# Optimization experiments

Hardware: AMD Instinct MI355X
Metric: run time of the kernel (lower is better)

The kernel has to match this reference:

```python
import jax, jax.numpy as jnp
import numpy as np

L, H, Q, D, N, DFF = 8, 4, 64, 512, 2048, 2048


def setup_inputs() -> dict:
    key = jax.random.key(0)
    ks = jax.random.split(key, 7)
    # Scale params by ~1/sqrt(fan_in) so the 8-layer residual stack stays numerically sane.
    X = jax.random.normal(ks[0], (D, N), dtype=jnp.float32)
    K = jax.random.normal(ks[1], (L, H, Q, D), dtype=jnp.float32) * (1.0 / np.sqrt(D))
    V = jax.random.normal(ks[2], (L, H, D, D), dtype=jnp.float32) * (0.5 / np.sqrt(D))
    W1 = jax.random.normal(ks[3], (L, DFF, D), dtype=jnp.float32) * (1.0 / np.sqrt(D))
    b1 = jax.random.normal(ks[4], (L, DFF, 1), dtype=jnp.float32) * 0.02
    W2 = jax.random.normal(ks[5], (L, D, DFF), dtype=jnp.float32) * (1.0 / np.sqrt(DFF))
    b2 = jax.random.normal(ks[6], (L, D, 1), dtype=jnp.float32) * 0.02
    return {"X": X, "K": K, "V": V, "W1": W1, "b1": b1, "W2": W2, "b2": b2}


def _argmax_attn_all_heads(Kl, Vl, X):
    # Kl: [H,Q,D], Vl: [H,D,D], X: [D,N]
    KX = jnp.einsum('hqd,dn->hqn', Kl, X)                 # [H,Q,N]
    scores = jnp.einsum('hqn,hqm->hnm', KX, KX)           # [H,N,N]
    max_vals = jnp.max(scores, axis=2, keepdims=True)     # [H,N,1]
    mask = (scores >= max_vals - 0.5).astype(X.dtype)     # hard argmax-threshold mask
    row_sums = jnp.maximum(jnp.sum(mask, axis=2, keepdims=True), 1.0)
    active = (jnp.abs(max_vals) > 0.5).astype(X.dtype)
    weights = (mask / row_sums) * active                  # [H,N,N]
    Xw = jnp.einsum('dn,hnm->hdm', X, weights)            # X @ weights per head
    return jnp.einsum('hde,hem->dm', Vl, Xw)              # sum over heads of V @ (X @ weights)


def reference(X, K, V, W1, b1, W2, b2):
    for li in range(L):
        attn = X + _argmax_attn_all_heads(K[li], V[li], X)
        ff1 = jax.nn.relu(W1[li] @ attn + b1[li])
        X = attn + W2[li] @ ff1 + b2[li]
    return X
```

## Files before the change

kernel.cpp:

```cpp
#include <hip/hip_runtime.h>

#define LL   8
#define HH   4
#define QQ   64
#define DD   512
#define NN   2048
#define DFFC 2048
#define ENTRY_CAP (1 << 17)
#define CHUNK 8
#define APPLY_BLOCKS 2048
#define LCAP 2048

typedef short     bf16x8 __attribute__((ext_vector_type(8)));
typedef float     f32x4  __attribute__((ext_vector_type(4)));
typedef unsigned short u16;

__device__ inline void splitf(float v, u16& h, u16& l)
{
    unsigned u  = __float_as_uint(v);
    unsigned uh = u + (0x7FFFu + ((u >> 16) & 1u));
    h = (u16)(uh >> 16);
    float fh = __uint_as_float(((unsigned)h) << 16);
    float r  = v - fh;
    unsigned ur = __float_as_uint(r);
    unsigned ul = ur + (0x7FFFu + ((ur >> 16) & 1u));
    l = (u16)(ul >> 16);
}

__device__ inline unsigned mapf(float f)
{
    unsigned u = __float_as_uint(f);
    return (u >> 31) ? ~u : (u | 0x80000000u);
}
__device__ inline float unmapf(unsigned u)
{
    return (u >> 31) ? __uint_as_float(u ^ 0x80000000u) : __uint_as_float(~u);
}

template <int BIAS, int RELU, int WF32, int WSPLIT>
__global__ __launch_bounds__(512, 2) void mgemm8_k(
    const u16* __restrict__ Ahi, const u16* __restrict__ Alo,
    const u16* __restrict__ Bhi, const u16* __restrict__ Blo,
    float* __restrict__ C, u16* __restrict__ Chi, u16* __restrict__ Clo,
    const float* __restrict__ bias,
    int K, int lda, int ldb, int ldc,
    long sAoff, long sBoff, long sCoff)
{
    __shared__ __align__(16) u16 smem[2 * 2048 * 8];

    const int bz = blockIdx.z;
    Ahi += bz * sAoff;  Alo += bz * sAoff;
    Bhi += bz * sBoff;  Blo += bz * sBoff;
    const long cOff = (long)bz * sCoff;

    const int gx = gridDim.x, nwg = gx * gridDim.y;
    int lin = blockIdx.y * gx + blockIdx.x;
    lin = (lin & 7) * (nwg >> 3) + (lin >> 3);
    const int bx = lin % gx, by = lin / gx;

    const int tid  = threadIdx.x;
    const int lane = tid & 63;
    const int wave = tid >> 6;
    const int quad = lane >> 4, l15 = lane & 15;
    const int wy = wave >> 1, wx = wave & 1;
    const long mTile = (long)by * 128;
    const long nTile = (long)bx * 128;

    const int fsw = (l15 & 3) ^ ((l15 >> 2) & 3);
    const int cA  = (quad ^ fsw) * 8;

    const int sr = tid >> 2;
    const int sc = (tid & 3) ^ ((sr & 3) ^ ((sr >> 2) & 3));
    const long aoff = (mTile + sr) * (long)lda + sc * 8;
    const long boff = (nTile + sr) * (long)ldb + sc * 8;

#define STAGE8(bufi, koff)                                                    \
    {                                                                         \
        u16* lb = (u16*)smem + (bufi) * (2048 * 8) + tid * 8;                 \
        __builtin_amdgcn_global_load_lds(                                     \
            (const __attribute__((address_space(1))) void*)(Ahi + aoff + (koff)), \
            (__attribute__((address_space(3))) void*)(lb), 16, 0, 0);         \
        __builtin_amdgcn_global_load_lds(                                     \
            (const __attribute__((address_space(1))) void*)(Alo + aoff + (koff)), \
            (__attribute__((address_space(3))) void*)(lb + 512 * 8), 16, 0, 0); \
        __builtin_amdgcn_global_load_lds(                                     \
            (const __attribute__((address_space(1))) void*)(Bhi + boff + (koff)), \
            (__attribute__((address_space(3))) void*)(lb + 1024 * 8), 16, 0, 0); \
        __builtin_amdgcn_global_load_lds(                                     \
            (const __attribute__((address_space(1))) void*)(Blo + boff + (koff)), \
            (__attribute__((address_space(3))) void*)(lb + 1536 * 8), 16, 0, 0); \
    }

    f32x4 acc[2][4];
#pragma unroll
    for (int i = 0; i < 2; i++)
#pragma unroll
        for (int j = 0; j < 4; j++)
            acc[i][j] = (f32x4){0.f, 0.f, 0.f, 0.f};

    STAGE8(0, 0)
    int buf = 0;
    const int NT = K >> 5;
    for (int t = 0; t < NT; t++) {
        __syncthreads();
        if (t + 1 < NT) STAGE8(buf ^ 1, (t + 1) << 5)

        const u16* Lb = (const u16*)smem + buf * (2048 * 8);
        bf16x8 ah[2], al[2], bh[4], bl[4];
#pragma unroll
        for (int i = 0; i < 2; i++) {
            const int off = (wy * 32 + i * 16 + l15) * 32 + cA;
            ah[i] = *(const bf16x8*)(Lb + off);
            al[i] = *(const bf16x8*)(Lb + 512 * 8 + off);
        }
#pragma unroll
        for (int j = 0; j < 4; j++) {
            const int off = (wx * 64 + j * 16 + l15) * 32 + cA;
            bh[j] = *(const bf16x8*)(Lb + 1024 * 8 + off);
            bl[j] = *(const bf16x8*)(Lb + 1536 * 8 + off);
        }

#pragma unroll
        for (int i = 0; i < 2; i++)
#pragma unroll
            for (int j = 0; j < 4; j++) {
                acc[i][j] = __builtin_amdgcn_mfma_f32_16x16x32_bf16(
                    ah[i], bh[j], acc[i][j], 0, 0, 0);
                acc[i][j] = __builtin_amdgcn_mfma_f32_16x16x32_bf16(
                    ah[i], bl[j], acc[i][j], 0, 0, 0);
                acc[i][j] = __builtin_amdgcn_mfma_f32_16x16x32_bf16(
                    al[i], bh[j], acc[i][j], 0, 0, 0);
            }
        buf ^= 1;
    }
#undef STAGE8

    const int mBase = (int)mTile + wy * 32;
    const int nBase = (int)nTile + wx * 64;
#pragma unroll
    for (int i = 0; i < 2; i++) {
#pragma unroll
        for (int j = 0; j < 4; j++) {
            const int n = nBase + j * 16 + l15;
            const float bv = BIAS ? bias[n] : 0.0f;
#pragma unroll
            for (int r = 0; r < 4; r++) {
                const int m = mBase + i * 16 + quad * 4 + r;
                float v = acc[i][j][r] + bv;
                if (RELU) v = fmaxf(v, 0.0f);
                const long o = cOff + (long)m * ldc + n;
                if (WF32) C[o] = v;
                if (WSPLIT) {
                    u16 h, l;
                    splitf(v, h, l);
                    Chi[o] = h;
                    Clo[o] = l;
                }
            }
        }
    }
}

template <int MI, int BIAS, int RELU, int WF32, int WSPLIT>
__global__ __launch_bounds__(256, 2) void mgemm_k(
    const u16* __restrict__ Ahi, const u16* __restrict__ Alo,
    const u16* __restrict__ Bhi, const u16* __restrict__ Blo,
    float* __restrict__ C, u16* __restrict__ Chi, u16* __restrict__ Clo,
    const float* __restrict__ bias,
    int M, int N, int K, int lda, int ldb, int ldc,
    long sAoff, long sBoff, long sCoff)
{
    constexpr int ACH = MI * 128;
    constexpr int TOT = 2 * ACH + 1024;
    __shared__ __align__(16) u16 smem[2 * TOT * 8];

    const int bz = blockIdx.z;
    Ahi += bz * sAoff;  Alo += bz * sAoff;
    Bhi += bz * sBoff;  Blo += bz * sBoff;
    const long cOff = (long)bz * sCoff;

    const int gx = gridDim.x, nwg = gx * gridDim.y;
    int lin = blockIdx.y * gx + blockIdx.x;
    lin = (lin & 7) * (nwg >> 3) + (lin >> 3);
    const int bxs = lin % gx, bys = lin / gx;

    const int tid  = threadIdx.x;
    const int wave = tid >> 6, lane = tid & 63;
    const int quad = lane >> 4, l15 = lane & 15;
    const int wy = wave >> 1, wx = wave & 1;
    const long mTile = (long)bys * (MI * 32);
    const long nTile = (long)bxs * 128;
    const int mBase = (int)mTile + wy * (MI * 16);
    const int nBase = (int)nTile + wx * 64;

    const int fsw = (l15 & 3) ^ ((l15 >> 2) & 3);
    const int cA  = (quad ^ fsw) * 8;

#define STAGE(bufi, koff)                                                     \
    {                                                                         \
        _Pragma("unroll")                                                     \
        for (int s = 0; s < TOT / 256; s++) {                                 \
            const int idx = s * 256 + tid;                                    \
            const u16* sp;  long rowb;  int ldx;  int rel;                    \
            if (idx < ACH)                { sp = Ahi; rel = idx;               rowb = 0; ldx = lda; } \
            else if (idx < 2 * ACH)       { sp = Alo; rel = idx - ACH;         rowb = 0; ldx = lda; } \
            else if (idx < 2 * ACH + 512) { sp = Bhi; rel = idx - 2 * ACH;     rowb = 1; ldx = ldb; } \
            else                          { sp = Blo; rel = idx - 2*ACH - 512; rowb = 1; ldx = ldb; } \
            const long rb = rowb ? nTile : mTile;                             \
            const int r = rel >> 2;                                           \
            const int c = (rel & 3) ^ ((r & 3) ^ ((r >> 2) & 3));             \
            const u16* g = sp + (rb + r) * (long)ldx + (koff) + c * 8;        \
            u16* lp = (u16*)smem + (bufi) * (TOT * 8) + idx * 8;              \
            __builtin_amdgcn_global_load_lds(                                 \
                (const __attribute__((address_space(1))) void*)g,             \
                (__attribute__((address_space(3))) void*)lp, 16, 0, 0);       \
        }                                                                     \
    }

    f32x4 acc[MI][4];
#pragma unroll
    for (int i = 0; i < MI; i++)
#pragma unroll
        for (int j = 0; j < 4; j++)
            acc[i][j] = (f32x4){0.f, 0.f, 0.f, 0.f};

    STAGE(0, 0)
    int buf = 0;
    const int NT = K >> 5;
    for (int t = 0; t < NT; t++) {
        __syncthreads();
        if (t + 1 < NT) STAGE(buf ^ 1, (t + 1) << 5)

        const u16* Lb = (const u16*)smem + buf * (TOT * 8);
        bf16x8 ah[MI], al[MI], bh[4], bl[4];
#pragma unroll
        for (int i = 0; i < MI; i++) {
            const int off = (wy * (MI * 16) + i * 16 + l15) * 32 + cA;
            ah[i] = *(const bf16x8*)(Lb + off);
            al[i] = *(const bf16x8*)(Lb + ACH * 8 + off);
        }
#pragma unroll
        for (int j = 0; j < 4; j++) {
            const int off = (wx * 64 + j * 16 + l15) * 32 + cA;
            bh[j] = *(const bf16x8*)(Lb + 2 * ACH * 8 + off);
            bl[j] = *(const bf16x8*)(Lb + 2 * ACH * 8 + 512 * 8 + off);
        }

#pragma unroll
        for (int i = 0; i < MI; i++)
#pragma unroll
            for (int j = 0; j < 4; j++) {
                acc[i][j] = __builtin_amdgcn_mfma_f32_16x16x32_bf16(
                    ah[i], bh[j], acc[i][j], 0, 0, 0);
                acc[i][j] = __builtin_amdgcn_mfma_f32_16x16x32_bf16(
                    ah[i], bl[j], acc[i][j], 0, 0, 0);
                acc[i][j] = __builtin_amdgcn_mfma_f32_16x16x32_bf16(
                    al[i], bh[j], acc[i][j], 0, 0, 0);
            }
        buf ^= 1;
    }
#undef STAGE

#pragma unroll
    for (int i = 0; i < MI; i++) {
#pragma unroll
        for (int j = 0; j < 4; j++) {
            const int n = nBase + j * 16 + l15;
            const float bv = BIAS ? bias[n] : 0.0f;
#pragma unroll
            for (int r = 0; r < 4; r++) {
                const int m = mBase + i * 16 + quad * 4 + r;
                float v = acc[i][j][r] + bv;
                if (RELU) v = fmaxf(v, 0.0f);
                const long o = cOff + (long)m * ldc + n;
                if (WF32) C[o] = v;
                if (WSPLIT) {
                    u16 h, l;
                    splitf(v, h, l);
                    Chi[o] = h;
                    Clo[o] = l;
                }
            }
        }
    }
}

__global__ __launch_bounds__(256, 2) void smax_k(
    const u16* __restrict__ Ghi, const u16* __restrict__ Glo,
    unsigned* __restrict__ rowmaxU, unsigned* __restrict__ tmaxU)
{
    __shared__ __align__(16) u16 gs[4096 * 8];
    const int h = blockIdx.z;
    const int lda = HH * QQ;
    const u16* Gh = Ghi + h * QQ;
    const u16* Gl = Glo + h * QQ;

    const int gx = gridDim.x, nwg = gx * gridDim.y;
    int lin = blockIdx.y * gx + blockIdx.x;
    lin = (lin & 7) * (nwg >> 3) + (lin >> 3);
    const int bxs = lin % gx, bys = lin / gx;

    const int tid  = threadIdx.x;
    const int wave = tid >> 6, lane = tid & 63;
    const int quad = lane >> 4, l15 = lane & 15;
    const int wy = wave >> 1, wx = wave & 1;
    const int rT = bys * 128, cT = bxs * 128;
    const int rB = rT + wy * 64;

#define SSTG(src, rowbase, dstbase)                                           \
    _Pragma("unroll")                                                         \
    for (int it = 0; it < 4; it++) {                                          \
        const int idx = it * 256 + tid;                                       \
        const int r = idx >> 3;                                               \
        const int c = (idx & 7) ^ (r & 7);                                    \
        __builtin_amdgcn_global_load_lds(                                     \
            (const __attribute__((address_space(1))) void*)(src + (long)((rowbase) + r) * lda + c * 8), \
            (__attribute__((address_space(3))) void*)((u16*)gs + (dstbase) + idx * 8), 16, 0, 0); \
    }
    SSTG(Gh, rT, 0)
    SSTG(Gl, rT, 8192)
    SSTG(Gh, cT, 16384)
    SSTG(Gl, cT, 24576)
#undef SSTG
    __syncthreads();

    bf16x8 ah[2][4], al[2][4], bh[2][4], bl[2][4];
#pragma unroll
    for (int s = 0; s < 2; s++) {
#pragma unroll
        for (int i = 0; i < 4; i++) {
            const int ra = wy * 64 + i * 16 + l15;
            const int ca = ((s * 4 + quad) ^ (ra & 7)) * 8;
            ah[s][i] = *(const bf16x8*)(gs + ra * 64 + ca);
            al[s][i] = *(const bf16x8*)(gs + 8192 + ra * 64 + ca);
            const int rb = wx * 64 + i * 16 + l15;
            const int cb = ((s * 4 + quad) ^ (rb & 7)) * 8;
            bh[s][i] = *(const bf16x8*)(gs + 16384 + rb * 64 + cb);
            bl[s][i] = *(const bf16x8*)(gs + 24576 + rb * 64 + cb);
        }
    }

    f32x4 acc[4][4];
#pragma unroll
    for (int i = 0; i < 4; i++)
#pragma unroll
        for (int j = 0; j < 4; j++)
            acc[i][j] = (f32x4){0.f, 0.f, 0.f, 0.f};

#pragma unroll
    for (int s = 0; s < 2; s++)
#pragma unroll
        for (int i = 0; i < 4; i++)
#pragma unroll
            for (int j = 0; j < 4; j++) {
                acc[i][j] = __builtin_amdgcn_mfma_f32_16x16x32_bf16(ah[s][i], bh[s][j], acc[i][j], 0, 0, 0);
                acc[i][j] = __builtin_amdgcn_mfma_f32_16x16x32_bf16(ah[s][i], bl[s][j], acc[i][j], 0, 0, 0);
                acc[i][j] = __builtin_amdgcn_mfma_f32_16x16x32_bf16(al[s][i], bh[s][j], acc[i][j], 0, 0, 0);
            }

    const unsigned tBase = (unsigned)((((h << 4) + bys) << 4) + bxs) * 128u;
#pragma unroll
    for (int i = 0; i < 4; i++)
#pragma unroll
        for (int r = 0; r < 4; r++) {
            float mx = acc[i][0][r];
#pragma unroll
            for (int j = 1; j < 4; j++) mx = fmaxf(mx, acc[i][j][r]);
#pragma unroll
            for (int off = 1; off < 16; off <<= 1)
                mx = fmaxf(mx, __shfl_xor(mx, off, 64));
            if (l15 == 0) {
                const int lr = wy * 64 + i * 16 + quad * 4 + r;
                const unsigned mv = mapf(mx);
                atomicMax(&rowmaxU[h * NN + rT + lr], mv);
                atomicMax(&tmaxU[tBase + lr], mv);
            }
        }
}

__global__ __launch_bounds__(256) void sextract_k(
    const u16* __restrict__ Ghi, const u16* __restrict__ Glo,
    const unsigned* __restrict__ rowmaxU, const unsigned* __restrict__ tmaxU,
    int* __restrict__ rowcnt,
    unsigned int* __restrict__ entries, int* __restrict__ counter)
{
    const int h = blockIdx.z;
    const u16* Ah = Ghi + h * QQ;
    const u16* Al = Glo + h * QQ;
    const int lda = HH * QQ;

    const int gx = gridDim.x, nwg = gx * gridDim.y;
    int lin = blockIdx.y * gx + blockIdx.x;
    lin = (lin & 7) * (nwg >> 3) + (lin >> 3);
    const int bxs = lin % gx, bys = lin / gx;

    const int tid  = threadIdx.x;
    const int wave = tid >> 6, lane = tid & 63;
    const int quad = lane >> 4, l15 = lane & 15;
    const int wy = wave >> 1, wx = wave & 1;
    const int rB = bys * 128 + wy * 64;
    const int cB = bxs * 128 + wx * 64;

    __shared__ float thrS[128];
    __shared__ unsigned lbuf[LCAP];
    __shared__ int lcnt, gbase, anyf;
    if (tid == 0) { lcnt = 0; anyf = 0; }
    if (tid < 128) {
        float mx = unmapf(rowmaxU[h * NN + bys * 128 + tid]);
        float thr = (fabsf(mx) > 0.5f) ? mx - 0.5f : 3.402823466e38f;
        thrS[tid] = thr;
        float tm = unmapf(tmaxU[(unsigned)((((h << 4) + bys) << 4) + bxs) * 128u + tid]);
        if (tm >= thr) atomicAdd(&anyf, 1);
    }
    __syncthreads();
    if (anyf == 0) return;

    bf16x8 ah[2][4], al[2][4], bh[2][4], bl[2][4];
#pragma unroll
    for (int s = 0; s < 2; s++) {
        const int kk = s * 32 + quad * 8;
#pragma unroll
        for (int i = 0; i < 4; i++) {
            long ar = (long)(rB + i * 16 + l15) * lda + kk;
            ah[s][i] = *(const bf16x8*)(Ah + ar);
            al[s][i] = *(const bf16x8*)(Al + ar);
            long br = (long)(cB + i * 16 + l15) * lda + kk;
            bh[s][i] = *(const bf16x8*)(Ah + br);
            bl[s][i] = *(const bf16x8*)(Al + br);
        }
    }

    f32x4 acc[4][4];
#pragma unroll
    for (int i = 0; i < 4; i++)
#pragma unroll
        for (int j = 0; j < 4; j++)
            acc[i][j] = (f32x4){0.f, 0.f, 0.f, 0.f};

#pragma unroll
    for (int s = 0; s < 2; s++)
#pragma unroll
        for (int i = 0; i < 4; i++)
#pragma unroll
            for (int j = 0; j < 4; j++) {
                acc[i][j] = __builtin_amdgcn_mfma_f32_16x16x32_bf16(ah[s][i], bh[s][j], acc[i][j], 0, 0, 0);
                acc[i][j] = __builtin_amdgcn_mfma_f32_16x16x32_bf16(ah[s][i], bl[s][j], acc[i][j], 0, 0, 0);
                acc[i][j] = __builtin_amdgcn_mfma_f32_16x16x32_bf16(al[s][i], bh[s][j], acc[i][j], 0, 0, 0);
            }

#pragma unroll
    for (int i = 0; i < 4; i++) {
#pragma unroll
        for (int r = 0; r < 4; r++) {
            const int lr  = wy * 64 + i * 16 + quad * 4 + r;
            const int row = h * NN + rB + i * 16 + quad * 4 + r;
            const float thr = thrS[lr];

            int c = 0;
#pragma unroll
            for (int j = 0; j < 4; j++) c += (acc[i][j][r] >= thr) ? 1 : 0;
            int cs = c;
#pragma unroll
            for (int off = 1; off < 16; off <<= 1) cs += __shfl_xor(cs, off, 64);
            if (l15 == 0 && cs > 0) atomicAdd(&rowcnt[row], cs);

#pragma unroll
            for (int j = 0; j < 4; j++) {
                if (acc[i][j][r] >= thr) {
                    unsigned ent = ((unsigned)row << 11) |
                                   (unsigned)(cB + j * 16 + l15);
                    int s2 = atomicAdd(&lcnt, 1);
                    if (s2 < LCAP) {
                        lbuf[s2] = ent;
                    } else {
                        unsigned p = (unsigned)atomicAdd(counter, 1);
                        if (p < ENTRY_CAP) entries[p] = ent;
                    }
                }
            }
        }
    }

    __syncthreads();
    int n = lcnt;
    if (n > LCAP) n = LCAP;
    if (n > 0) {
        if (tid == 0) gbase = atomicAdd(counter, n);
        __syncthreads();
        for (int i2 = tid; i2 < n; i2 += 256) {
            unsigned p = (unsigned)(gbase + i2);
            if (p < ENTRY_CAP) entries[p] = lbuf[i2];
        }
    }
}

__global__ __launch_bounds__(256) void split_k(
    const float* __restrict__ src, u16* __restrict__ hi, u16* __restrict__ lo)
{
    int i = blockIdx.x * 256 + threadIdx.x;
    float4 v = ((const float4*)src)[i];
    ushort4 hv, lv;
    splitf(v.x, hv.x, lv.x);
    splitf(v.y, hv.y, lv.y);
    splitf(v.z, hv.z, lv.z);
    splitf(v.w, hv.w, lv.w);
    ((ushort4*)hi)[i] = hv;
    ((ushort4*)lo)[i] = lv;
}

__global__ __launch_bounds__(256) void splitc_k(
    const float* __restrict__ src, u16* __restrict__ hi, u16* __restrict__ lo,
    float* __restrict__ cpy)
{
    int i = blockIdx.x * 256 + threadIdx.x;
    float4 v = ((const float4*)src)[i];
    ((float4*)cpy)[i] = v;
    ushort4 hv, lv;
    splitf(v.x, hv.x, lv.x);
    splitf(v.y, hv.y, lv.y);
    splitf(v.z, hv.z, lv.z);
    splitf(v.w, hv.w, lv.w);
    ((ushort4*)hi)[i] = hv;
    ((ushort4*)lo)[i] = lv;
}

__global__ __launch_bounds__(256) void splitw_k(
    const float* __restrict__ K_, const float* __restrict__ V_,
    const float* __restrict__ W1_, const float* __restrict__ W2_,
    u16* __restrict__ Khi, u16* __restrict__ Klo,
    u16* __restrict__ Vhi, u16* __restrict__ Vlo,
    u16* __restrict__ W1hi, u16* __restrict__ W1lo,
    u16* __restrict__ W2hi, u16* __restrict__ W2lo,
    unsigned* __restrict__ zrow, unsigned* __restrict__ ztmax)
{
    int i = blockIdx.x * 256 + threadIdx.x;
    if (i < 16384) zrow[i] = 0u;
    if (i < 131072) ztmax[i] = 0u;
    const float* s;
    u16 *h, *l;
    int off;
    if (i < 32768)       { s = K_;  h = Khi;  l = Klo;  off = i; }
    else if (i < 294912) { s = V_;  h = Vhi;  l = Vlo;  off = i - 32768; }
    else if (i < 557056) { s = W1_; h = W1hi; l = W1lo; off = i - 294912; }
    else                 { s = W2_; h = W2hi; l = W2lo; off = i - 557056; }
    float4 v = ((const float4*)s)[off];
    ushort4 hv, lv;
    splitf(v.x, hv.x, lv.x);
    splitf(v.y, hv.y, lv.y);
    splitf(v.z, hv.z, lv.z);
    splitf(v.w, hv.w, lv.w);
    ((ushort4*)h)[off] = hv;
    ((ushort4*)l)[off] = lv;
}

__global__ void zero_k(int* __restrict__ counters)
{
    if (threadIdx.x < LL) counters[threadIdx.x] = 0;
}

__global__ __launch_bounds__(256) void buildcsr_k(
    const unsigned int* __restrict__ entries, const int* __restrict__ counter,
    unsigned int* __restrict__ csr, int* __restrict__ colOff)
{
    __shared__ int hist[NN];
    __shared__ int part[256];
    const int t = threadIdx.x;
    int cnt = *counter;
    if (cnt > ENTRY_CAP) cnt = ENTRY_CAP;

    for (int i = t; i < NN; i += 256) hist[i] = 0;
    __syncthreads();
    for (int i = t; i < cnt; i += 256)
        atomicAdd(&hist[entries[i] & 2047], 1);
    __syncthreads();

    int e[8];
    int s = 0;
#pragma unroll
    for (int i = 0; i < 8; i++) { e[i] = s; s += hist[t * 8 + i]; }
    part[t] = s;
    __syncthreads();
    for (int off = 1; off < 256; off <<= 1) {
        int x = (t >= off) ? part[t - off] : 0;
        __syncthreads();
        part[t] += x;
        __syncthreads();
    }
    int base = (t > 0) ? part[t - 1] : 0;
    int my[8];
#pragma unroll
    for (int i = 0; i < 8; i++) my[i] = base + e[i];
#pragma unroll
    for (int i = 0; i < 8; i++) colOff[t * 8 + i] = my[i];
    if (t == 255) colOff[NN] = part[255];
    __syncthreads();
#pragma unroll
    for (int i = 0; i < 8; i++) hist[t * 8 + i] = my[i];
    __syncthreads();

    for (int i = t; i < cnt; i += 256) {
        unsigned v = entries[i];
        int slot = atomicAdd(&hist[v & 2047], 1);
        csr[slot] = v;
    }
}

__global__ __launch_bounds__(256) void apply_k(
    const unsigned int* __restrict__ csr, const int* __restrict__ colOff,
    const unsigned* __restrict__ rowmaxU, const int* __restrict__ rowcnt,
    const float* __restrict__ Yt, float* __restrict__ attnT)
{
    const int total = colOff[NN];
    const int tid = threadIdx.x;

    for (int base = blockIdx.x * CHUNK; base < total;
         base += gridDim.x * CHUNK) {
        int end = base + CHUNK;
        if (end > total) end = total;

        float a0 = 0.0f, a1 = 0.0f;
        int curM = -1;
        for (int e = base; e < end; e++) {
            unsigned v = csr[e];
            int m = v & 2047;
            int row = (int)(v >> 11);
            if (m != curM) {
                if (curM >= 0) {
                    atomicAdd(&attnT[(long)curM * DD + tid], a0);
                    atomicAdd(&attnT[(long)curM * DD + tid + 256], a1);
                }
                curM = m;
                a0 = a1 = 0.0f;
            }
            float mx = unmapf(rowmaxU[row]);
            float w = (fabsf(mx) > 0.5f)
                          ? 1.0f / fmaxf((float)rowcnt[row], 1.0f) : 0.0f;
            const float* y = Yt + (long)row * DD;
            a0 += w * y[tid];
            a1 += w * y[tid + 256];
        }
        if (curM >= 0) {
            atomicAdd(&attnT[(long)curM * DD + tid], a0);
            atomicAdd(&attnT[(long)curM * DD + tid + 256], a1);
        }
    }
}

__global__ __launch_bounds__(256) void ff2red_k(
    const float* __restrict__ Cpart, const float* __restrict__ b2,
    float* __restrict__ attnT, float* __restrict__ Xn,
    u16* __restrict__ Xhi, u16* __restrict__ Xlo)
{
    int i = blockIdx.x * 256 + threadIdx.x;
    float4 v0 = ((const float4*)(Cpart))[i];
    float4 v1 = ((const float4*)(Cpart + 1048576))[i];
    float4 v2 = ((const float4*)(Cpart + 2097152))[i];
    float4 v3 = ((const float4*)(Cpart + 3145728))[i];
    float4 bv = ((const float4*)b2)[i & 127];
    float4 rv = ((const float4*)attnT)[i];
    float4 o;
    o.x = v0.x + v1.x + v2.x + v3.x + bv.x + rv.x;
    o.y = v0.y + v1.y + v2.y + v3.y + bv.y + rv.y;
    o.z = v0.z + v1.z + v2.z + v3.z + bv.z + rv.z;
    o.w = v0.w + v1.w + v2.w + v3.w + bv.w + rv.w;
    ((float4*)Xn)[i] = o;
    ((float4*)attnT)[i] = o;
    ushort4 hv, lv;
    splitf(o.x, hv.x, lv.x);
    splitf(o.y, hv.y, lv.y);
    splitf(o.z, hv.z, lv.z);
    splitf(o.w, hv.w, lv.w);
    ((ushort4*)Xhi)[i] = hv;
    ((ushort4*)Xlo)[i] = lv;
}

__global__ __launch_bounds__(256) void transpose_k(
    const float* __restrict__ src, float* __restrict__ dst, int R, int C)
{
    __shared__ float t[32][33];
    int tx = threadIdx.x & 31, ty = threadIdx.x >> 5;
    int c0 = blockIdx.x * 32, r0 = blockIdx.y * 32;
#pragma unroll
    for (int k = 0; k < 4; k++)
        t[ty + 8 * k][tx] = src[(long)(r0 + ty + 8 * k) * C + c0 + tx];
    __syncthreads();
#pragma unroll
    for (int k = 0; k < 4; k++)
        dst[(long)(c0 + ty + 8 * k) * R + r0 + tx] = t[tx][ty + 8 * k];
}

extern "C" void kernel_launch(void* const* d_in, const int* in_sizes, int n_in,
                              void* d_out, int out_size, void* d_ws, size_t ws_size,
                              hipStream_t stream)
{
    const float* X0 = (const float*)d_in[0];
    const float* Kw = (const float*)d_in[1];
    const float* Vw = (const float*)d_in[2];
    const float* W1 = (const float*)d_in[3];
    const float* b1 = (const float*)d_in[4];
    const float* W2 = (const float*)d_in[5];
    const float* b2 = (const float*)d_in[6];
    float* out = (float*)d_out;

    float* R0    = (float*)d_ws;
    float* Yt    = R0;
    u16*   ff1hi = (u16*)(R0 + 4194304);
    u16*   ff1lo = (u16*)(R0 + 6291456);
    float* Cpart = R0 + 8388608;
    float* attnT = R0 + 12582912;

    float* ext = R0 + 13631488;
    u16* KXThi = (u16*)ext;
    u16* KXTlo = (u16*)(ext + 262144);
    float* XbufA = ext + 524288;
    float* XbufB = ext + 1572864;
    u16* Xhi  = (u16*)(ext + 2621440);
    u16* Xlo  = (u16*)(ext + 3145728);
    u16* athi = (u16*)(ext + 3670016);
    u16* atlo = (u16*)(ext + 4194304);
    u16* Khi  = (u16*)(ext + 4718592);
    u16* Klo  = (u16*)(ext + 4784128);
    u16* Vhi  = (u16*)(ext + 4849664);
    u16* Vlo  = (u16*)(ext + 5373952);
    u16* W1hi = (u16*)(ext + 5898240);
    u16* W1lo = (u16*)(ext + 6422528);
    u16* W2hi = (u16*)(ext + 6946816);
    u16* W2lo = (u16*)(ext + 7471104);
    unsigned int* entries = (unsigned int*)(ext + 8003584);
    unsigned int* csr     = (unsigned int*)(ext + 8134656);
    int* colOff   = (int*)(ext + 8265728);
    int* counters = (int*)(ext + 8267840);
    unsigned* rowmaxU = (unsigned*)(ext + 8267904);
    int* rowcnt   = (int*)(ext + 8276096);
    unsigned* tmaxU = (unsigned*)(ext + 8284288);

    zero_k<<<1, 64, 0, stream>>>(counters);

    transpose_k<<<dim3(NN / 32, DD / 32), 256, 0, stream>>>(X0, XbufA, DD, NN);
    splitc_k<<<dim3(1024), 256, 0, stream>>>(XbufA, Xhi, Xlo, attnT);

    float* Xc = XbufA;
    for (int li = 0; li < LL; li++) {
        float* Xn = (li & 1) ? XbufA : XbufB;

        splitw_k<<<dim3(3200), 256, 0, stream>>>(
            Kw + (long)li * 131072, Vw + (long)li * 1048576,
            W1 + (long)li * 1048576, W2 + (long)li * 1048576,
            Khi, Klo, Vhi, Vlo, W1hi, W1lo, W2hi, W2lo, rowmaxU, tmaxU);

        mgemm_k<1, 0, 0, 0, 1><<<dim3(2, 64, 1), 256, 0, stream>>>(
            Xhi, Xlo, Khi, Klo, nullptr, KXThi, KXTlo, nullptr,
            NN, HH * QQ, DD, DD, DD, HH * QQ, 0, 0, 0);

        smax_k<<<dim3(16, 16, HH), 256, 0, stream>>>(KXThi, KXTlo, rowmaxU, tmaxU);
        sextract_k<<<dim3(16, 16, HH), 256, 0, stream>>>(
            KXThi, KXTlo, rowmaxU, tmaxU, rowcnt, entries, counters + li);
        buildcsr_k<<<dim3(1), 256, 0, stream>>>(entries, counters + li, csr, colOff);

        mgemm8_k<0, 0, 1, 0><<<dim3(4, 16, HH), 512, 0, stream>>>(
            Xhi, Xlo, Vhi, Vlo, Yt, nullptr, nullptr, nullptr,
            DD, DD, DD, DD, 0, (long)DD * DD, (long)NN * DD);

        apply_k<<<dim3(APPLY_BLOCKS), 256, 0, stream>>>(
            csr, colOff, rowmaxU, rowcnt, Yt, attnT);
        split_k<<<dim3(1024), 256, 0, stream>>>(attnT, athi, atlo);

        mgemm8_k<1, 1, 0, 1><<<dim3(16, 16, 1), 512, 0, stream>>>(
            athi, atlo, W1hi, W1lo, nullptr, ff1hi, ff1lo,
            b1 + (long)li * DFFC,
            DD, DD, DD, DFFC, 0, 0, 0);

        mgemm8_k<0, 0, 1, 0><<<dim3(4, 16, 4), 512, 0, stream>>>(
            ff1hi, ff1lo, W2hi, W2lo, Cpart, nullptr, nullptr, nullptr,
            512, DFFC, DFFC, DD, 512, 512, (long)NN * DD);
        ff2red_k<<<dim3(1024), 256, 0, stream>>>(
            Cpart, b2 + (long)li * DD, attnT, Xn, Xhi, Xlo);

        Xc = Xn;
    }

    transpose_k<<<dim3(DD / 32, NN / 32), 256, 0, stream>>>(Xc, out, NN, DD);
}
```

Before: 1.362 ms.

## Parallelize CSR build, hoist weight splitting, fuse zeroing into KX gemm

Weights for all layers are split into bf16 hi/lo pairs in one upfront kernel instead of once per layer. Scratch zeroing is folded into the KX gemm. The single-block CSR build is replaced by a column histogram accumulated in the extraction kernel, a one-block scan, and a multi-block atomic scatter. This removes serialized per-layer kernels at the cost of extra global atomics, more workspace, and nondeterministic entry order within each column.

```diff
diff --git a/kernel.cpp b/kernel.cpp
--- a/kernel.cpp
+++ b/kernel.cpp
@@ -10,6 +10,7 @@
 #define CHUNK 8
 #define APPLY_BLOCKS 2048
 #define LCAP 2048
+#define ZWORDS 149504
 
 typedef short     bf16x8 __attribute__((ext_vector_type(8)));
 typedef float     f32x4  __attribute__((ext_vector_type(4)));
@@ -168,7 +169,8 @@
     float* __restrict__ C, u16* __restrict__ Chi, u16* __restrict__ Clo,
     const float* __restrict__ bias,
     int M, int N, int K, int lda, int ldb, int ldc,
-    long sAoff, long sBoff, long sCoff)
+    long sAoff, long sBoff, long sCoff,
+    unsigned* __restrict__ zbase, int zn)
 {
     constexpr int ACH = MI * 128;
     constexpr int TOT = 2 * ACH + 1024;
@@ -185,6 +187,13 @@
     const int bxs = lin % gx, bys = lin / gx;
 
     const int tid  = threadIdx.x;
+
+    if (zbase) {
+        const int gtid = (blockIdx.y * gx + blockIdx.x) * 256 + tid;
+        const int gstr = nwg * 256;
+        for (int i = gtid; i < zn; i += gstr) zbase[i] = 0u;
+    }
+
     const int wave = tid >> 6, lane = tid & 63;
     const int quad = lane >> 4, l15 = lane & 15;
     const int wy = wave >> 1, wx = wave & 1;
@@ -381,7 +390,7 @@
 __global__ __launch_bounds__(256) void sextract_k(
     const u16* __restrict__ Ghi, const u16* __restrict__ Glo,
     const unsigned* __restrict__ rowmaxU, const unsigned* __restrict__ tmaxU,
-    int* __restrict__ rowcnt,
+    int* __restrict__ rowcnt, unsigned* __restrict__ colcnt,
     unsigned int* __restrict__ entries, int* __restrict__ counter)
 {
     const int h = blockIdx.z;
@@ -467,8 +476,9 @@
 #pragma unroll
             for (int j = 0; j < 4; j++) {
                 if (acc[i][j][r] >= thr) {
-                    unsigned ent = ((unsigned)row << 11) |
-                                   (unsigned)(cB + j * 16 + l15);
+                    const unsigned m = (unsigned)(cB + j * 16 + l15);
+                    unsigned ent = ((unsigned)row << 11) | m;
+                    atomicAdd(&colcnt[m], 1u);
                     int s2 = atomicAdd(&lcnt, 1);
                     if (s2 < LCAP) {
                         lbuf[s2] = ent;
@@ -491,6 +501,47 @@
             unsigned p = (unsigned)(gbase + i2);
             if (p < ENTRY_CAP) entries[p] = lbuf[i2];
         }
+    }
+}
+
+__global__ __launch_bounds__(256) void scan_k(
+    const unsigned* __restrict__ colcnt, int* __restrict__ colOff,
+    int* __restrict__ colCur)
+{
+    __shared__ int part[256];
+    const int t = threadIdx.x;
+    int e[8];
+    int s = 0;
+#pragma unroll
+    for (int i = 0; i < 8; i++) { e[i] = s; s += (int)colcnt[t * 8 + i]; }
+    part[t] = s;
+    __syncthreads();
+    for (int off = 1; off < 256; off <<= 1) {
+        int x = (t >= off) ? part[t - off] : 0;
+        __syncthreads();
+        part[t] += x;
+        __syncthreads();
+    }
+    int base = (t > 0) ? part[t - 1] : 0;
+#pragma unroll
+    for (int i = 0; i < 8; i++) {
+        colOff[t * 8 + i] = base + e[i];
+        colCur[t * 8 + i] = base + e[i];
+    }
+    if (t == 255) colOff[NN] = part[255];
+}
+
+__global__ __launch_bounds__(256) void scatter_k(
+    const unsigned int* __restrict__ entries, const int* __restrict__ counter,
+    unsigned int* __restrict__ csr, int* __restrict__ colCur)
+{
+    int cnt = *counter;
+    if (cnt > ENTRY_CAP) cnt = ENTRY_CAP;
+    for (int i = blockIdx.x * 256 + threadIdx.x; i < cnt;
+         i += gridDim.x * 256) {
+        unsigned v = entries[i];
+        int slot = atomicAdd(&colCur[v & 2047], 1);
+        csr[slot] = v;
     }
 }
 
@@ -524,25 +575,37 @@
     ((ushort4*)lo)[i] = lv;
 }
 
-__global__ __launch_bounds__(256) void splitw_k(
+__global__ __launch_bounds__(256) void splitall_k(
     const float* __restrict__ K_, const float* __restrict__ V_,
     const float* __restrict__ W1_, const float* __restrict__ W2_,
-    u16* __restrict__ Khi, u16* __restrict__ Klo,
-    u16* __restrict__ Vhi, u16* __restrict__ Vlo,
-    u16* __restrict__ W1hi, u16* __restrict__ W1lo,
-    u16* __restrict__ W2hi, u16* __restrict__ W2lo,
-    unsigned* __restrict__ zrow, unsigned* __restrict__ ztmax)
-{
-    int i = blockIdx.x * 256 + threadIdx.x;
-    if (i < 16384) zrow[i] = 0u;
-    if (i < 131072) ztmax[i] = 0u;
+    u16* __restrict__ KhiA, u16* __restrict__ KloA,
+    u16* __restrict__ VhiA, u16* __restrict__ VloA,
+    u16* __restrict__ W1hiA, u16* __restrict__ W1loA,
+    u16* __restrict__ W2hiA, u16* __restrict__ W2loA)
+{
+    const int li  = blockIdx.x / 3200;
+    const int sub = blockIdx.x % 3200;
+    int i = sub * 256 + threadIdx.x;
     const float* s;
     u16 *h, *l;
     int off;
-    if (i < 32768)       { s = K_;  h = Khi;  l = Klo;  off = i; }
-    else if (i < 294912) { s = V_;  h = Vhi;  l = Vlo;  off = i - 32768; }
-    else if (i < 557056) { s = W1_; h = W1hi; l = W1lo; off = i - 294912; }
-    else                 { s = W2_; h = W2hi; l = W2lo; off = i - 557056; }
+    if (i < 32768) {
+        s = K_ + (long)li * 131072;
+        h = KhiA + (long)li * 131072;  l = KloA + (long)li * 131072;
+        off = i;
+    } else if (i < 294912) {
+        s = V_ + (long)li * 1048576;
+        h = VhiA + (long)li * 1048576; l = VloA + (long)li * 1048576;
+        off = i - 32768;
+    } else if (i < 557056) {
+        s = W1_ + (long)li * 1048576;
+        h = W1hiA + (long)li * 1048576; l = W1loA + (long)li * 1048576;
+        off = i - 294912;
+    } else {
+        s = W2_ + (long)li * 1048576;
+        h = W2hiA + (long)li * 1048576; l = W2loA + (long)li * 1048576;
+        off = i - 557056;
+    }
     float4 v = ((const float4*)s)[off];
     ushort4 hv, lv;
     splitf(v.x, hv.x, lv.x);
@@ -556,53 +619,6 @@
 __global__ void zero_k(int* __restrict__ counters)
 {
     if (threadIdx.x < LL) counters[threadIdx.x] = 0;
-}
-
-__global__ __launch_bounds__(256) void buildcsr_k(
-    const unsigned int* __restrict__ entries, const int* __restrict__ counter,
-    unsigned int* __restrict__ csr, int* __restrict__ colOff)
-{
-    __shared__ int hist[NN];
-    __shared__ int part[256];
-    const int t = threadIdx.x;
-    int cnt = *counter;
-    if (cnt > ENTRY_CAP) cnt = ENTRY_CAP;
-
-    for (int i = t; i < NN; i += 256) hist[i] = 0;
-    __syncthreads();
-    for (int i = t; i < cnt; i += 256)
-        atomicAdd(&hist[entries[i] & 2047], 1);
-    __syncthreads();
-
-    int e[8];
-    int s = 0;
-#pragma unroll
-    for (int i = 0; i < 8; i++) { e[i] = s; s += hist[t * 8 + i]; }
-    part[t] = s;
-    __syncthreads();
-    for (int off = 1; off < 256; off <<= 1) {
-        int x = (t >= off) ? part[t - off] : 0;
-        __syncthreads();
-        part[t] += x;
-        __syncthreads();
-    }
-    int base = (t > 0) ? part[t - 1] : 0;
-    int my[8];
-#pragma unroll
-    for (int i = 0; i < 8; i++) my[i] = base + e[i];
-#pragma unroll
-    for (int i = 0; i < 8; i++) colOff[t * 8 + i] = my[i];
-    if (t == 255) colOff[NN] = part[255];
-    __syncthreads();
-#pragma unroll
-    for (int i = 0; i < 8; i++) hist[t * 8 + i] = my[i];
-    __syncthreads();
-
-    for (int i = t; i < cnt; i += 256) {
-        unsigned v = entries[i];
-        int slot = atomicAdd(&hist[v & 2047], 1);
-        csr[slot] = v;
-    }
 }
 
 __global__ __launch_bounds__(256) void apply_k(
@@ -718,23 +734,29 @@
     u16* Xlo  = (u16*)(ext + 3145728);
     u16* athi = (u16*)(ext + 3670016);
     u16* atlo = (u16*)(ext + 4194304);
-    u16* Khi  = (u16*)(ext + 4718592);
-    u16* Klo  = (u16*)(ext + 4784128);
-    u16* Vhi  = (u16*)(ext + 4849664);
-    u16* Vlo  = (u16*)(ext + 5373952);
-    u16* W1hi = (u16*)(ext + 5898240);
-    u16* W1lo = (u16*)(ext + 6422528);
-    u16* W2hi = (u16*)(ext + 6946816);
-    u16* W2lo = (u16*)(ext + 7471104);
     unsigned int* entries = (unsigned int*)(ext + 8003584);
     unsigned int* csr     = (unsigned int*)(ext + 8134656);
     int* colOff   = (int*)(ext + 8265728);
     int* counters = (int*)(ext + 8267840);
     unsigned* rowmaxU = (unsigned*)(ext + 8267904);
     int* rowcnt   = (int*)(ext + 8276096);
-    unsigned* tmaxU = (unsigned*)(ext + 8284288);
+    unsigned* colcnt = (unsigned*)(ext + 8284288);
+    unsigned* tmaxU = (unsigned*)(ext + 8286336);
+    int* colCur   = (int*)(ext + 8417408);
+    u16* wbase = (u16*)(ext + 8419456);
+    u16* KhiA  = wbase;
+    u16* KloA  = wbase + 1048576;
+    u16* VhiA  = wbase + 2097152;
+    u16* VloA  = wbase + 10485760;
+    u16* W1hiA = wbase + 18874368;
+    u16* W1loA = wbase + 27262976;
+    u16* W2hiA = wbase + 35651584;
+    u16* W2loA = wbase + 44040192;
 
     zero_k<<<1, 64, 0, stream>>>(counters);
+
+    splitall_k<<<dim3(LL * 3200), 256, 0, stream>>>(
+        Kw, Vw, W1, W2, KhiA, KloA, VhiA, VloA, W1hiA, W1loA, W2hiA, W2loA);
 
     transpose_k<<<dim3(NN / 32, DD / 32), 256, 0, stream>>>(X0, XbufA, DD, NN);
     splitc_k<<<dim3(1024), 256, 0, stream>>>(XbufA, Xhi, Xlo, attnT);
@@ -742,20 +764,25 @@
     float* Xc = XbufA;
     for (int li = 0; li < LL; li++) {
         float* Xn = (li & 1) ? XbufA : XbufB;
-
-        splitw_k<<<dim3(3200), 256, 0, stream>>>(
-            Kw + (long)li * 131072, Vw + (long)li * 1048576,
-            W1 + (long)li * 1048576, W2 + (long)li * 1048576,
-            Khi, Klo, Vhi, Vlo, W1hi, W1lo, W2hi, W2lo, rowmaxU, tmaxU);
+        u16* Khi = KhiA + (long)li * 131072;
+        u16* Klo = KloA + (long)li * 131072;
+        u16* Vhi = VhiA + (long)li * 1048576;
+        u16* Vlo = VloA + (long)li * 1048576;
+        u16* W1hi = W1hiA + (long)li * 1048576;
+        u16* W1lo = W1loA + (long)li * 1048576;
+        u16* W2hi = W2hiA + (long)li * 1048576;
+        u16* W2lo = W2loA + (long)li * 1048576;
 
         mgemm_k<1, 0, 0, 0, 1><<<dim3(2, 64, 1), 256, 0, stream>>>(
             Xhi, Xlo, Khi, Klo, nullptr, KXThi, KXTlo, nullptr,
-            NN, HH * QQ, DD, DD, DD, HH * QQ, 0, 0, 0);
+            NN, HH * QQ, DD, DD, DD, HH * QQ, 0, 0, 0,
+            rowmaxU, ZWORDS);
 
         smax_k<<<dim3(16, 16, HH), 256, 0, stream>>>(KXThi, KXTlo, rowmaxU, tmaxU);
         sextract_k<<<dim3(16, 16, HH), 256, 0, stream>>>(
-            KXThi, KXTlo, rowmaxU, tmaxU, rowcnt, entries, counters + li);
-        buildcsr_k<<<dim3(1), 256, 0, stream>>>(entries, counters + li, csr, colOff);
+            KXThi, KXTlo, rowmaxU, tmaxU, rowcnt, colcnt, entries, counters + li);
+        scan_k<<<dim3(1), 256, 0, stream>>>(colcnt, colOff, colCur);
+        scatter_k<<<dim3(128), 256, 0, stream>>>(entries, counters + li, csr, colCur);
 
         mgemm8_k<0, 0, 1, 0><<<dim3(4, 16, HH), 512, 0, stream>>>(
             Xhi, Xlo, Vhi, Vlo, Yt, nullptr, nullptr, nullptr,
```

After: 1.798 ms. +32.1%, slower.
